# Kernel optimization log

Measured on AMD Instinct MI355X. Metric: run time of the kernel, lower is better.

Reference implementation:

```python
import jax, jax.numpy as jnp
import numpy as np

CD_STEPS = 1

def _sample_binary(p, u):
    # relu(sign(p - u)): 1.0 where p > u else 0.0
    return (p > u).astype(p.dtype)

def setup_inputs() -> dict:
    key = jax.random.key(0)
    k_v, k_w, k_vb, k_uh, k_uv = jax.random.split(key, 5)
    B, V, H = 8192, 2048, 1024
    return {
        "v": jax.random.uniform(k_v, (B, V), dtype=jnp.float32),
        "w": jax.random.normal(k_w, (V, H), dtype=jnp.float32) * 0.01,
        "vb": jax.random.normal(k_vb, (V,), dtype=jnp.float32) * 0.01,
        "hb": jnp.zeros((H,), dtype=jnp.float32),
        "u_h": jax.random.uniform(k_uh, (CD_STEPS + 1, B, H), dtype=jnp.float32),
        "u_v": jax.random.uniform(k_uv, (CD_STEPS, B, V), dtype=jnp.float32),
    }

def reference(v, w, vb, hb, u_h, u_v):
    sig = jax.nn.sigmoid
    # mean-field forward
    h_p = sig(hb + v @ w)                     # [B,H]
    h_prediction = h_p
    v_prediction = sig(vb + h_p @ w.T)        # [B,V]
    reconstruction_error = jnp.mean(jnp.mean(jnp.abs(v - v_prediction), axis=1))
    # data statistics
    h = _sample_binary(h_p, u_h[0])           # [B,H]
    vb_data_grad = jnp.sum(v, axis=0)
    hb_data_grad = jnp.sum(h_p, axis=0)
    # sum_b outer(v_b, h_b) == v^T @ h (original materialized [B,V,H])
    w_data_grad = jnp.einsum('bv,bh->vh', v, h)
    # CD-k chain
    vk = v
    for k in range(CD_STEPS):
        vk = _sample_binary(sig(vb + h @ w.T), u_v[k])
        h = _sample_binary(sig(hb + vk @ w), u_h[k + 1])
    vb_model_grad = jnp.sum(vk, axis=0)
    hb_model_grad = jnp.sum(h, axis=0)
    w_model_grad = jnp.einsum('bv,bh->vh', vk, h)
    vb_grad = vb_model_grad - vb_data_grad
    hb_grad = hb_model_grad - hb_data_grad
    w_grad = w_model_grad - w_data_grad
    return h_prediction, reconstruction_error, w_grad, vb_grad, hb_grad
```

## Files before the change

kernel.cpp:

```cpp
#include <hip/hip_runtime.h>


typedef unsigned short u16;
typedef short s16x8 __attribute__((ext_vector_type(8)));
typedef float f32x4 __attribute__((ext_vector_type(4)));
typedef u16 u16x4 __attribute__((ext_vector_type(4)));
typedef u16 u16x8 __attribute__((ext_vector_type(8)));

constexpr int Bn = 8192, Vn = 2048, Hn = 1024;
constexpr size_t VH = (size_t)Vn * Hn;
constexpr size_t BH = (size_t)Bn * Hn;
constexpr size_t OUT_RECON = BH;
constexpr size_t OUT_WGRAD = OUT_RECON + 1;
constexpr size_t OUT_VBG   = OUT_WGRAD + VH;
constexpr size_t OUT_HBG   = OUT_VBG + Vn;

__device__ __forceinline__ u16 f2bf(float x) {
  union { float f; unsigned u; } a; a.f = x;
  unsigned r = a.u + 0x7FFFu + ((a.u >> 16) & 1u);
  return (u16)(r >> 16);
}
__device__ __forceinline__ float bf2f(u16 h) {
  union { unsigned u; float f; } a; a.u = ((unsigned)h) << 16;
  return a.f;
}
__device__ __forceinline__ float sigmoidf_(float x) {
  return 1.0f / (1.0f + expf(-x));
}

using gptr_t = const unsigned int __attribute__((address_space(1)))*;
using lptr_t = unsigned int __attribute__((address_space(3)))*;

__device__ __forceinline__ void gload16(const u16* g, u16* l) {
  __builtin_amdgcn_global_load_lds((gptr_t)(unsigned long long)g,
                                   (lptr_t)(unsigned long long)l, 16, 0, 0);
}


__global__ void prep_vt_k(const float* __restrict__ v, u16* __restrict__ vcat,
                          u16* __restrict__ vT, float* __restrict__ vbd_p) {
  __shared__ u16 tile[64][68];
  __shared__ float cs[16][64];
  const int b0 = blockIdx.x * 64, c0 = blockIdx.y * 64;
  const int t = threadIdx.x;
  const int rg = t >> 4;
  const int cg = (t & 15) << 2;
  float ca[4] = {0.f, 0.f, 0.f, 0.f};
#pragma unroll
  for (int i = 0; i < 4; ++i) {
    int r = rg + 16 * i;
    f32x4 x = *(const f32x4*)&v[(size_t)(b0 + r) * Vn + c0 + cg];
    u16x4 hi, lo;
#pragma unroll
    for (int j = 0; j < 4; ++j) {
      hi[j] = f2bf(x[j]);
      lo[j] = f2bf(x[j] - bf2f(hi[j]));
      tile[r][cg + j] = hi[j];
      ca[j] += x[j];
    }
    *(u16x4*)&vcat[(size_t)(b0 + r) * (2 * Vn) + c0 + cg] = hi;
    *(u16x4*)&vcat[(size_t)(b0 + r) * (2 * Vn) + Vn + c0 + cg] = lo;
  }
#pragma unroll
  for (int j = 0; j < 4; ++j) cs[rg][cg + j] = ca[j];
  __syncthreads();
  if (t < 64) {
    float s = 0.f;
#pragma unroll
    for (int k = 0; k < 16; ++k) s += cs[k][t];
    vbd_p[(size_t)blockIdx.x * Vn + c0 + t] = s;
  }
#pragma unroll
  for (int s2 = 0; s2 < 2; ++s2) {
    int c = t >> 2;
    int seg = (t & 3) + 4 * s2;
    u16x8 pk;
#pragma unroll
    for (int i = 0; i < 8; ++i) pk[i] = tile[seg * 8 + i][c];
    *(u16x8*)&vT[(size_t)(c0 + c) * Bn + b0 + seg * 8] = pk;
  }
}

__global__ void prep_w_k(const float* __restrict__ w, u16* __restrict__ w_cat,
                         u16* __restrict__ wTc) {
  __shared__ float tile[64][65];
  int v0 = blockIdx.x * 64, h0 = blockIdx.y * 64;
  int t = threadIdx.x, c = t & 63, r = t >> 6;
  for (int rr = r; rr < 64; rr += 4) {
    float x = w[(size_t)(v0 + rr) * Hn + h0 + c];
    tile[rr][c] = x;
    u16 hi = f2bf(x), lo = f2bf(x - bf2f(hi));
    w_cat[(size_t)(v0 + rr) * (2 * Hn) + h0 + c]      = hi;
    w_cat[(size_t)(v0 + rr) * (2 * Hn) + Hn + h0 + c] = lo;
  }
  __syncthreads();
  for (int rr = r; rr < 64; rr += 4) {
    float x = tile[c][rr];
    u16 hi = f2bf(x), lo = f2bf(x - bf2f(hi));
    size_t ro = (size_t)(h0 + rr) * (2 * Vn);
    wTc[ro + v0 + c]      = hi;
    wTc[ro + Vn + v0 + c] = lo;
  }
}

template <int M>
__global__ void epi_h_k(const float* __restrict__ p0, const float* __restrict__ p1,
                        const float* __restrict__ bias, const float* __restrict__ uni,
                        float* __restrict__ f32out, u16* __restrict__ hp_out,
                        u16* __restrict__ hbin_out, u16* __restrict__ tout,
                        float* __restrict__ colp) {
  __shared__ u16 tile[64][68];
  __shared__ float cs[16][64];
  const int b0 = blockIdx.x * 64, c0 = blockIdx.y * 64;
  const int t = threadIdx.x;
  const int rg = t >> 4, cg = (t & 15) << 2;
  float ca[4] = {0.f, 0.f, 0.f, 0.f};
#pragma unroll
  for (int i = 0; i < 4; ++i) {
    int r = rg + 16 * i;
    size_t e = (size_t)(b0 + r) * Hn + c0 + cg;
    f32x4 a = *(const f32x4*)&p0[e];
    f32x4 b = *(const f32x4*)&p1[e];
    f32x4 uu = *(const f32x4*)&uni[e];
    f32x4 hpv;
    u16x4 hb16, qv;
#pragma unroll
    for (int j = 0; j < 4; ++j) {
      float hp = sigmoidf_(a[j] + b[j] + bias[c0 + cg + j]);
      u16 qb = (hp > uu[j]) ? (u16)0x3F80 : (u16)0;
      tile[r][cg + j] = qb;
      if constexpr (M == 1) {
        hpv[j] = hp; hb16[j] = f2bf(hp); qv[j] = qb;
        ca[j] += hp;
      } else {
        ca[j] += (qb ? 1.f : 0.f);
      }
    }
    if constexpr (M == 1) {
      *(f32x4*)&f32out[e] = hpv;
      *(u16x4*)&hp_out[e] = hb16;
      *(u16x4*)&hbin_out[e] = qv;
    }
  }
#pragma unroll
  for (int j = 0; j < 4; ++j) cs[rg][cg + j] = ca[j];
  __syncthreads();
  if (t < 64) {
    float s = 0.f;
#pragma unroll
    for (int k = 0; k < 16; ++k) s += cs[k][t];
    colp[(size_t)blockIdx.x * Hn + c0 + t] = s;
  }
#pragma unroll
  for (int s2 = 0; s2 < 2; ++s2) {
    int c = t >> 2;
    int seg = (t & 3) + 4 * s2;
    u16x8 pk;
#pragma unroll
    for (int i = 0; i < 8; ++i) pk[i] = tile[seg * 8 + i][c];
    *(u16x8*)&tout[(size_t)(c0 + c) * Bn + b0 + seg * 8] = pk;
  }
}

template <int MODE>
__global__ __launch_bounds__(512) void gemm256(
    const u16* __restrict__ A, int lda, const u16* __restrict__ Bm, int ldb, int K,
    const float* __restrict__ bias, const float* __restrict__ uni,
    const float* __restrict__ aux, float* __restrict__ f32out,
    u16* __restrict__ bfout, u16* __restrict__ bfout2,
    float* __restrict__ redp, u16* __restrict__ tout, float* __restrict__ colp) {
  constexpr bool TRANS = (MODE == 4);
  __shared__ __align__(16) u16 smem[TRANS ? 67584 : 65536];
  const int t = threadIdx.x;
  const int lane = t & 63, wave = t >> 6;
  const int wr = (wave >> 2) << 7;
  const int wc = (wave & 3) << 6;
  const int bm = blockIdx.x << 8, bn = blockIdx.y << 8;
  int kbeg = 0;
  float* pout = f32out;
  if constexpr (MODE == 1 || MODE == 5) {
    kbeg = blockIdx.z * K;
    pout = (blockIdx.z == 0) ? f32out : redp;
  }
  if constexpr (MODE == 3) {
    size_t off = (size_t)blockIdx.z * (size_t)K;
    A += off;
    Bm += off;
    pout = ((blockIdx.z < 4) ? f32out : redp) + (size_t)(blockIdx.z & 3) * VH;
  }
  f32x4 acc[8][4] = {};
  const int sr = t >> 2;
  const int sc = (((t & 3) ^ ((t >> 3) & 3)) << 3);
  const u16* Ag  = A  + (size_t)(bm + sr) * lda + sc;
  const u16* Ag2 = Ag + (size_t)128 * lda;
  const u16* Bg  = Bm + (size_t)(bn + sr) * ldb + sc;
  const u16* Bg2 = Bg + (size_t)128 * ldb;
  const int fr = lane & 15, fg = lane >> 4;
  const int ga = ((fg ^ ((fr >> 1) & 3)) << 3);

  auto stage = [&](int kt) {
    const int k0 = kbeg + (kt << 5);
    int acol, bcol;
    if constexpr (MODE == 1) {
      acol = (k0 < 2048) ? k0 : k0 - 2048;
      bcol = (k0 < 4096) ? k0 : k0 - 4096;
    } else if constexpr (MODE == 4) { acol = k0 & 1023; bcol = k0; }
    else if constexpr (MODE == 5)   { acol = k0 & 2047; bcol = k0; }
    else                            { acol = k0;        bcol = k0; }
    const int pb = kt & 3;
    u16* ad = smem + pb * 8192 + wave * 512;
    u16* bd = smem + 32768 + pb * 8192 + wave * 512;
    gload16(Ag + acol, ad);
    gload16(Ag2 + acol, ad + 4096);
    gload16(Bg + bcol, bd);
    gload16(Bg2 + bcol, bd + 4096);
  };
  auto compute = [&](int kt) {
    const int pb = kt & 3;
    const u16* Ab = smem + pb * 8192;
    const u16* Bb = smem + 32768 + pb * 8192;
    s16x8 bf[4], af[4];
#pragma unroll
    for (int n = 0; n < 4; ++n)
      bf[n] = *(const s16x8*)&Bb[(wc + n * 16 + fr) * 32 + ga];
#pragma unroll
    for (int m = 0; m < 4; ++m)
      af[m] = *(const s16x8*)&Ab[(wr + m * 16 + fr) * 32 + ga];
    __builtin_amdgcn_s_setprio(1);
#pragma unroll
    for (int m = 0; m < 4; ++m)
#pragma unroll
      for (int n = 0; n < 4; ++n)
        acc[m][n] = __builtin_amdgcn_mfma_f32_16x16x32_bf16(af[m], bf[n], acc[m][n], 0, 0, 0);
    __builtin_amdgcn_s_setprio(0);
#pragma unroll
    for (int m = 0; m < 4; ++m)
      af[m] = *(const s16x8*)&Ab[(wr + (m + 4) * 16 + fr) * 32 + ga];
    __builtin_amdgcn_s_setprio(1);
#pragma unroll
    for (int m = 0; m < 4; ++m)
#pragma unroll
      for (int n = 0; n < 4; ++n)
        acc[m + 4][n] = __builtin_amdgcn_mfma_f32_16x16x32_bf16(af[m], bf[n], acc[m + 4][n], 0, 0, 0);
    __builtin_amdgcn_s_setprio(0);
  };

  const int NT = K >> 5;
  stage(0); stage(1); stage(2);
  int T = 0;
  for (; T < NT - 3; ++T) {
    asm volatile("s_waitcnt vmcnt(8)" ::: "memory");
    __builtin_amdgcn_s_barrier();
    asm volatile("" ::: "memory");
    stage(T + 3);
    compute(T);
  }
  asm volatile("s_waitcnt vmcnt(8)" ::: "memory");
  __builtin_amdgcn_s_barrier();
  asm volatile("" ::: "memory");
  compute(T++);
  asm volatile("s_waitcnt vmcnt(4)" ::: "memory");
  __builtin_amdgcn_s_barrier();
  asm volatile("" ::: "memory");
  compute(T++);
  asm volatile("s_waitcnt vmcnt(0)" ::: "memory");
  __builtin_amdgcn_s_barrier();
  asm volatile("" ::: "memory");
  compute(T);

  constexpr int NC = (MODE == 2 || MODE == 4) ? Vn : Hn;
  const int fq = lane >> 4;
  float lsum = 0.f;
  float csum[4] = {0.f, 0.f, 0.f, 0.f};
  if constexpr (TRANS) __syncthreads();

#pragma unroll
  for (int m = 0; m < 8; ++m) {
#pragma unroll
    for (int n = 0; n < 4; ++n) {
#pragma unroll
      for (int j = 0; j < 4; ++j) {
        int rl = wr + m * 16 + fq * 4 + j;
        int cl = wc + n * 16 + fr;
        int row = bm + rl, col = bn + cl;
        float a = acc[m][n][j];
        size_t e = (size_t)row * NC + col;
        if constexpr (MODE == 1 || MODE == 3 || MODE == 5) {
          pout[e] = a;
        } else if constexpr (MODE == 2) {
          float vp = sigmoidf_(a + bias[col]);
          lsum += fabsf(aux[e] - vp);
        } else if constexpr (MODE == 4) {
          float vp = sigmoidf_(a + bias[col]);
          u16 qb = (vp > uni[e]) ? (u16)0x3F80 : (u16)0;
          bfout[e] = qb;
          smem[rl * 264 + cl] = qb;
          csum[n] += (qb ? 1.f : 0.f);
        }
      }
    }
  }

  if constexpr (TRANS) {
#pragma unroll
    for (int n = 0; n < 4; ++n) {
      float s = csum[n];
      s += __shfl_xor(s, 16);
      s += __shfl_xor(s, 32);
      if (fq == 0)
        colp[(size_t)(blockIdx.x * 2 + (wr >> 7)) * NC + (bn + wc + n * 16 + fr)] = s;
    }
    __syncthreads();
#pragma unroll
    for (int it = 0; it < 16; ++it) {
      int id = t + (it << 9);
      int c = id & 255;
      int rg2 = id >> 8;
      u16x8 pk;
#pragma unroll
      for (int i2 = 0; i2 < 8; ++i2) pk[i2] = smem[(rg2 * 8 + i2) * 264 + c];
      *(u16x8*)&tout[(size_t)(bn + c) * Bn + bm + rg2 * 8] = pk;
    }
  }

  if constexpr (MODE == 2) {
#pragma unroll
    for (int off = 32; off > 0; off >>= 1) lsum += __shfl_down(lsum, off);
    __syncthreads();
    float* redlds = (float*)smem;
    if (lane == 0) redlds[wave] = lsum;
    __syncthreads();
    if (t == 0) {
      float s = 0.f;
#pragma unroll
      for (int wv = 0; wv < 8; ++wv) s += redlds[wv];
      redp[(size_t)blockIdx.y * gridDim.x + blockIdx.x] = s;
    }
  }
}

__global__ void reduce8_k(const float* __restrict__ p, float* __restrict__ out) {
  size_t e = ((size_t)blockIdx.x * 256 + threadIdx.x) * 4;
  f32x4 r = {};
#pragma unroll
  for (int z = 0; z < 8; ++z) r += *(const f32x4*)&p[(size_t)z * VH + e];
  out[e + 0] = r[0]; out[e + 1] = r[1]; out[e + 2] = r[2]; out[e + 3] = r[3];
}

__global__ void reduce8s_k(const float* __restrict__ pa, const float* __restrict__ pb,
                           const float* __restrict__ sub, float* __restrict__ out) {
  size_t e = ((size_t)blockIdx.x * 256 + threadIdx.x) * 4;
  f32x4 r = {};
#pragma unroll
  for (int z = 0; z < 4; ++z) r += *(const f32x4*)&pa[(size_t)z * VH + e];
#pragma unroll
  for (int z = 0; z < 4; ++z) r += *(const f32x4*)&pb[(size_t)z * VH + e];
  float s0 = sub[e + 0], s1 = sub[e + 1], s2 = sub[e + 2], s3 = sub[e + 3];
  out[e + 0] = r[0] - s0; out[e + 1] = r[1] - s1;
  out[e + 2] = r[2] - s2; out[e + 3] = r[3] - s3;
}

__global__ void finalize_k(const float* __restrict__ sums, float* __restrict__ out) {
  int i = blockIdx.x * 256 + threadIdx.x;
  const float* recon_p = sums;
  const float* vbd = sums + 1024;
  const float* hbd = vbd + 128 * 2048;
  const float* vbm = hbd + 128 * 1024;
  const float* hbm = vbm + 128 * 2048;
  if (i < 2048) {
    float d = 0.f, m = 0.f;
    for (int k = 0; k < 128; ++k) d += vbd[k * 2048 + i];
    for (int k = 0; k < 64; ++k)  m += vbm[k * 2048 + i];
    out[OUT_VBG + i] = m - d;
  }
  if (i < 1024) {
    float d = 0.f, m = 0.f;
    for (int k = 0; k < 128; ++k) { d += hbd[k * 1024 + i]; m += hbm[k * 1024 + i]; }
    out[OUT_HBG + i] = m - d;
  }
  if (i == 0) {
    float s = 0.f;
    for (int k = 0; k < 256; ++k) s += recon_p[k];
    out[OUT_RECON] = s * (1.0f / 16777216.0f);
  }
}

extern "C" void kernel_launch(void* const* d_in, const int* in_sizes, int n_in,
                              void* d_out, int out_size, void* d_ws, size_t ws_size,
                              hipStream_t stream) {
  (void)in_sizes; (void)n_in; (void)out_size;
  const float* v   = (const float*)d_in[0];
  const float* w   = (const float*)d_in[1];
  const float* vb  = (const float*)d_in[2];
  const float* hb  = (const float*)d_in[3];
  const float* u_h = (const float*)d_in[4];
  const float* u_v = (const float*)d_in[5];
  float* out = (float*)d_out;
  char* ws = (char*)d_ws;
  if (ws_size < 204734464ULL) return;

  float* sums    = (float*)ws;
  float* recon_p = sums;
  float* vbd_p   = sums + 1024;
  float* hbd_p   = vbd_p + 128 * 2048;
  float* vbm_p   = hbd_p + 128 * 1024;
  float* hbm_p   = vbm_p + 128 * 2048;
  char* p = ws + 3407872;
  u16* v_cat  = (u16*)p;  p += (size_t)Bn * 2 * Vn * 2;
  u16* wT_cat = (u16*)p;  p += (size_t)Hn * 2 * Vn * 2;
  u16* w_cat  = (u16*)p;  p += (size_t)Vn * 2 * Hn * 2;
  u16* h_p    = (u16*)p;  p += BH * 2;
  u16* hbin   = (u16*)p;  p += BH * 2;
  u16* vT     = (u16*)p;  p += (size_t)Vn * Bn * 2;
  u16* hT     = (u16*)p;  p += (size_t)Hn * Bn * 2;
  float* big  = (float*)p;
  u16* vk   = v_cat;
  u16* vkT  = vT;
  u16* h2T  = hT;
  float* vcat_f = (float*)v_cat;
  float* hpbuf  = (float*)h_p;
  float* outW   = out + OUT_WGRAD;

  prep_vt_k<<<dim3(Bn / 64, Vn / 64), 256, 0, stream>>>(v, v_cat, vT, vbd_p);
  prep_w_k<<<dim3(Vn / 64, Hn / 64), 256, 0, stream>>>(w, w_cat, wT_cat);
  gemm256<1><<<dim3(32, 4, 2), 512, 0, stream>>>(
      v_cat, 2 * Vn, wT_cat, 2 * Vn, 3072, nullptr, nullptr, nullptr,
      out, nullptr, nullptr, big, nullptr, nullptr);
  epi_h_k<1><<<dim3(128, 16), 256, 0, stream>>>(
      out, big, hb, u_h, out, h_p, hbin, hT, hbd_p);
  gemm256<2><<<dim3(32, 8), 512, 0, stream>>>(
      h_p, Hn, w_cat, 2 * Hn, Hn, vb, nullptr, v,
      nullptr, nullptr, nullptr, recon_p, nullptr, nullptr);
  gemm256<3><<<dim3(Vn / 256, Hn / 256, 8), 512, 0, stream>>>(
      vT, Bn, hT, Bn, 1024, nullptr, nullptr, nullptr,
      vcat_f, nullptr, nullptr, vcat_f + 4 * VH, nullptr, nullptr);
  reduce8_k<<<2048, 256, 0, stream>>>(vcat_f, outW);
  gemm256<4><<<dim3(32, 8), 512, 0, stream>>>(
      hbin, Hn, w_cat, 2 * Hn, 2 * Hn, vb, u_v, nullptr,
      nullptr, vk, nullptr, nullptr, vkT, vbm_p);
  gemm256<5><<<dim3(32, 4, 2), 512, 0, stream>>>(
      vk, Vn, wT_cat, 2 * Vn, 2048, nullptr, nullptr, nullptr,
      hpbuf, nullptr, nullptr, big, nullptr, nullptr);
  epi_h_k<5><<<dim3(128, 16), 256, 0, stream>>>(
      hpbuf, big, hb, u_h + BH, nullptr, nullptr, nullptr, h2T, hbm_p);
  gemm256<3><<<dim3(Vn / 256, Hn / 256, 8), 512, 0, stream>>>(
      vkT, Bn, h2T, Bn, 1024, nullptr, nullptr, nullptr,
      hpbuf, nullptr, nullptr, big, nullptr, nullptr);
  reduce8s_k<<<2048, 256, 0, stream>>>(hpbuf, big, outW, outW);
  finalize_k<<<8, 256, 0, stream>>>(sums, out);
}
```

Baseline: 556.9 us.

## Prefetch epilogue operands, software-pipeline epilogue loads, vectorize sampled-bit stores

In the V-side GEMM epilogues, the last main-loop iterations now issue dummy loads of the aux/uniform tile so it is warm in cache when the epilogue runs. The epilogue is rewritten to apply the sigmoid to all accumulators first, then stream aux/uniform values through a rolling 8-slot register buffer. The bf16 sample output is now written row-wise from LDS with 16-byte stores instead of scattered 2-byte stores, and sigmoid uses the fast __expf. This targets epilogue memory latency and store inefficiency, at the cost of extra loads, more registers and slightly less accurate exp.

Measured after the change: 526.6 us. -5.4%, faster.

```diff
diff --git a/kernel.cpp b/kernel.cpp
--- a/kernel.cpp
+++ b/kernel.cpp
@@ -25,7 +25,7 @@
   return a.f;
 }
 __device__ __forceinline__ float sigmoidf_(float x) {
-  return 1.0f / (1.0f + expf(-x));
+  return 1.0f / (1.0f + __expf(-x));
 }
 
 using gptr_t = const unsigned int __attribute__((address_space(1)))*;
@@ -253,6 +253,15 @@
     __builtin_amdgcn_s_barrier();
     asm volatile("" ::: "memory");
     stage(T + 3);
+    if constexpr (MODE == 2 || MODE == 4) {
+      const int pfbeg = NT - 11;
+      if (T >= pfbeg) {
+        const float* pfp = (MODE == 2) ? aux : uni;
+        const int L = ((T - pfbeg) << 9) + t;
+        float pf = pfp[(size_t)(bm + (L >> 4)) * Vn + bn + ((L & 15) << 4)];
+        asm volatile("" :: "v"(pf));
+      }
+    }
     compute(T);
   }
   asm volatile("s_waitcnt vmcnt(8)" ::: "memory");
@@ -270,60 +279,48 @@
 
   constexpr int NC = (MODE == 2 || MODE == 4) ? Vn : Hn;
   const int fq = lane >> 4;
-  float lsum = 0.f;
-  float csum[4] = {0.f, 0.f, 0.f, 0.f};
-  if constexpr (TRANS) __syncthreads();
-
-#pragma unroll
-  for (int m = 0; m < 8; ++m) {
-#pragma unroll
-    for (int n = 0; n < 4; ++n) {
-#pragma unroll
-      for (int j = 0; j < 4; ++j) {
-        int rl = wr + m * 16 + fq * 4 + j;
-        int cl = wc + n * 16 + fr;
-        int row = bm + rl, col = bn + cl;
-        float a = acc[m][n][j];
-        size_t e = (size_t)row * NC + col;
-        if constexpr (MODE == 1 || MODE == 3 || MODE == 5) {
-          pout[e] = a;
-        } else if constexpr (MODE == 2) {
-          float vp = sigmoidf_(a + bias[col]);
-          lsum += fabsf(aux[e] - vp);
-        } else if constexpr (MODE == 4) {
-          float vp = sigmoidf_(a + bias[col]);
-          u16 qb = (vp > uni[e]) ? (u16)0x3F80 : (u16)0;
-          bfout[e] = qb;
-          smem[rl * 264 + cl] = qb;
-          csum[n] += (qb ? 1.f : 0.f);
+
+  if constexpr (MODE == 1 || MODE == 3 || MODE == 5) {
+#pragma unroll
+    for (int m = 0; m < 8; ++m)
+#pragma unroll
+      for (int n = 0; n < 4; ++n)
+#pragma unroll
+        for (int j = 0; j < 4; ++j) {
+          int rl = wr + m * 16 + fq * 4 + j;
+          int cl = wc + n * 16 + fr;
+          pout[(size_t)(bm + rl) * NC + bn + cl] = acc[m][n][j];
         }
-      }
-    }
-  }
-
-  if constexpr (TRANS) {
-#pragma unroll
-    for (int n = 0; n < 4; ++n) {
-      float s = csum[n];
-      s += __shfl_xor(s, 16);
-      s += __shfl_xor(s, 32);
-      if (fq == 0)
-        colp[(size_t)(blockIdx.x * 2 + (wr >> 7)) * NC + (bn + wc + n * 16 + fr)] = s;
-    }
-    __syncthreads();
-#pragma unroll
-    for (int it = 0; it < 16; ++it) {
-      int id = t + (it << 9);
-      int c = id & 255;
-      int rg2 = id >> 8;
-      u16x8 pk;
-#pragma unroll
-      for (int i2 = 0; i2 < 8; ++i2) pk[i2] = smem[(rg2 * 8 + i2) * 264 + c];
-      *(u16x8*)&tout[(size_t)(bn + c) * Bn + bm + rg2 * 8] = pk;
-    }
   }
 
   if constexpr (MODE == 2) {
+    float bcol[4];
+#pragma unroll
+    for (int n = 0; n < 4; ++n) bcol[n] = bias[bn + wc + n * 16 + fr];
+    const size_t ebase = (size_t)(bm + wr + fq * 4) * NC + (bn + wc + fr);
+    float ax[8][4];
+    auto ld4 = [&](int ci, float* dst) {
+      size_t e0 = ebase + (size_t)((ci >> 2) << 4) * NC + ((ci & 3) << 4);
+      dst[0] = aux[e0];          dst[1] = aux[e0 + NC];
+      dst[2] = aux[e0 + 2 * NC]; dst[3] = aux[e0 + 3 * NC];
+    };
+#pragma unroll
+    for (int ci = 0; ci < 8; ++ci) ld4(ci, ax[ci]);
+#pragma unroll
+    for (int m = 0; m < 8; ++m)
+#pragma unroll
+      for (int n = 0; n < 4; ++n)
+#pragma unroll
+        for (int j = 0; j < 4; ++j)
+          acc[m][n][j] = sigmoidf_(acc[m][n][j] + bcol[n]);
+    float lsum = 0.f;
+#pragma unroll
+    for (int ci = 0; ci < 32; ++ci) {
+      const int m = ci >> 2, n = ci & 3;
+#pragma unroll
+      for (int j = 0; j < 4; ++j) lsum += fabsf(ax[ci & 7][j] - acc[m][n][j]);
+      if (ci < 24) ld4(ci + 8, ax[ci & 7]);
+    }
 #pragma unroll
     for (int off = 32; off > 0; off >>= 1) lsum += __shfl_down(lsum, off);
     __syncthreads();
@@ -335,6 +332,70 @@
 #pragma unroll
       for (int wv = 0; wv < 8; ++wv) s += redlds[wv];
       redp[(size_t)blockIdx.y * gridDim.x + blockIdx.x] = s;
+    }
+  }
+
+  if constexpr (MODE == 4) {
+    __syncthreads();
+    float bcol[4];
+#pragma unroll
+    for (int n = 0; n < 4; ++n) bcol[n] = bias[bn + wc + n * 16 + fr];
+    const size_t ebase = (size_t)(bm + wr + fq * 4) * NC + (bn + wc + fr);
+    float ux[8][4];
+    auto ld4 = [&](int ci, float* dst) {
+      size_t e0 = ebase + (size_t)((ci >> 2) << 4) * NC + ((ci & 3) << 4);
+      dst[0] = uni[e0];          dst[1] = uni[e0 + NC];
+      dst[2] = uni[e0 + 2 * NC]; dst[3] = uni[e0 + 3 * NC];
+    };
+#pragma unroll
+    for (int ci = 0; ci < 8; ++ci) ld4(ci, ux[ci]);
+#pragma unroll
+    for (int m = 0; m < 8; ++m)
+#pragma unroll
+      for (int n = 0; n < 4; ++n)
+#pragma unroll
+        for (int j = 0; j < 4; ++j)
+          acc[m][n][j] = sigmoidf_(acc[m][n][j] + bcol[n]);
+    float csum[4] = {0.f, 0.f, 0.f, 0.f};
+#pragma unroll
+    for (int ci = 0; ci < 32; ++ci) {
+      const int m = ci >> 2, n = ci & 3;
+      const int rl = wr + m * 16 + fq * 4;
+      const int cl = wc + n * 16 + fr;
+#pragma unroll
+      for (int j = 0; j < 4; ++j) {
+        u16 qb = (acc[m][n][j] > ux[ci & 7][j]) ? (u16)0x3F80 : (u16)0;
+        smem[(rl + j) * 264 + cl] = qb;
+        csum[n] += (qb ? 1.f : 0.f);
+      }
+      if (ci < 24) ld4(ci + 8, ux[ci & 7]);
+    }
+#pragma unroll
+    for (int n = 0; n < 4; ++n) {
+      float s = csum[n];
+      s += __shfl_xor(s, 16);
+      s += __shfl_xor(s, 32);
+      if (fq == 0)
+        colp[(size_t)(blockIdx.x * 2 + (wr >> 7)) * NC + (bn + wc + n * 16 + fr)] = s;
+    }
+    __syncthreads();
+#pragma unroll
+    for (int it = 0; it < 16; ++it) {
+      int id = t + (it << 9);
+      int r = id >> 5;
+      int c0 = (id & 31) << 3;
+      u16x8 pk = *(const u16x8*)&smem[r * 264 + c0];
+      *(u16x8*)&bfout[(size_t)(bm + r) * NC + bn + c0] = pk;
+    }
+#pragma unroll
+    for (int it = 0; it < 16; ++it) {
+      int id = t + (it << 9);
+      int c = id & 255;
+      int rg2 = id >> 8;
+      u16x8 pk;
+#pragma unroll
+      for (int i2 = 0; i2 < 8; ++i2) pk[i2] = smem[(rg2 * 8 + i2) * 264 + c];
+      *(u16x8*)&tout[(size_t)(bn + c) * Bn + bm + rg2 * 8] = pk;
     }
   }
 }
```
